# Kernel optimization log

Measured on AMD Instinct MI355X. Metric: run time of the kernel, lower is better.

Reference implementation:

```python
import jax, jax.numpy as jnp
import numpy as np

HEADS = 4
DIM_HEAD = 32
DIM = 256
EPS = 1e-12


def setup_inputs() -> dict:
    key = jax.random.key(0)
    ks = jax.random.split(key, 4)
    b, c, n = 8, DIM, 16384
    hidden = HEADS * DIM_HEAD  # 128
    x = jax.random.normal(ks[0], (b, c, n), dtype=jnp.float32)
    w_qkv = jax.random.normal(ks[1], (hidden * 3, c), dtype=jnp.float32) * (1.0 / np.sqrt(c))
    w_out = jax.random.normal(ks[2], (c, hidden), dtype=jnp.float32) * (1.0 / np.sqrt(hidden))
    b_out = jax.random.normal(ks[3], (c,), dtype=jnp.float32) * 0.01
    g = jnp.ones((1, c, 1), dtype=jnp.float32)
    return {"x": x, "w_qkv": w_qkv, "w_out": w_out, "b_out": b_out, "g": g}


def reference(x, w_qkv, w_out, b_out, g):
    b, c, n = x.shape
    scale = DIM_HEAD ** -0.5
    # to_qkv: Conv1d kernel-size 1, no bias == channel matmul
    qkv = jnp.einsum('oc,bcn->bon', w_qkv, x)  # [b, 3*h*d, n]
    q, k, v = jnp.split(qkv, 3, axis=1)
    def to_heads(t):
        return t.reshape(b, HEADS, DIM_HEAD, n)  # b (h d) n -> b h d n
    q, k, v = to_heads(q), to_heads(k), to_heads(v)
    q = jax.nn.softmax(q, axis=-2) * scale      # softmax over d
    k = jax.nn.softmax(k, axis=-1)              # softmax over n
    context = jnp.einsum('bhdn,bhen->bhde', k, v)  # [b,h,d,e]
    out = jnp.einsum('bhde,bhdn->bhen', context, q)  # [b,h,e,n]
    out = out.reshape(b, HEADS * DIM_HEAD, n)   # b h d n -> b (h d) n
    # to_out Conv1d (kernel 1) with bias
    out = jnp.einsum('oc,bcn->bon', w_out, out) + b_out[None, :, None]
    # RMSNorm: F.normalize over channel dim * g * sqrt(c)
    norm = jnp.sqrt(jnp.sum(out * out, axis=1, keepdims=True))
    out = out / jnp.maximum(norm, EPS) * g * jnp.sqrt(jnp.asarray(c, out.dtype))
    return out
```

## Files before the change

kernel.cpp:

```cpp
#include <hip/hip_runtime.h>
#include <hip/hip_bf16.h>
#include <math.h>

#define B_    8
#define C_    256
#define N_    16384
#define H_    4
#define D_    32
#define HID_  128
#define ROWS_ 384
#define SCALE 0.17677669529663687f

typedef __attribute__((ext_vector_type(8))) short bf16x8;
typedef __attribute__((ext_vector_type(16))) float f32x16;

__device__ __forceinline__ short f2bf(float f) {
    union { __hip_bfloat16 h; short s; } u;
    u.h = __float2bfloat16(f);
    return u.s;
}
__device__ __forceinline__ float bf2f(short s) {
    union { unsigned u; float f; } x;
    x.u = ((unsigned)(unsigned short)s) << 16;
    return x.f;
}

__global__ __launch_bounds__(256) void k_conv(
    const float* __restrict__ wqkv, const float* __restrict__ wout,
    short* __restrict__ wrearr, short* __restrict__ woutb)
{
    int i = blockIdx.x * 256 + threadIdx.x;
    if (i < 12288) {
        int tile = i >> 10;
        int ks   = (i >> 6) & 15;
        int l    = i & 63;
        int row  = tile * 32 + (l & 31);
        int k0   = ks * 16 + (l >> 5) * 8;
        const float* src = wqkv + row * 256 + k0;
        float4 f0 = *(const float4*)(src);
        float4 f1 = *(const float4*)(src + 4);
        short o[8] = {f2bf(f0.x), f2bf(f0.y), f2bf(f0.z), f2bf(f0.w),
                      f2bf(f1.x), f2bf(f1.y), f2bf(f1.z), f2bf(f1.w)};
        *(uint4*)(wrearr + (size_t)i * 8) = *(uint4*)o;
    } else {
        int j = (i - 12288) * 4;
        float4 f = *(const float4*)(wout + j);
        short4 s; s.x = f2bf(f.x); s.y = f2bf(f.y); s.z = f2bf(f.z); s.w = f2bf(f.w);
        *(short4*)(woutb + j) = s;
    }
}

__global__ __launch_bounds__(512, 4) void k_qkv(
    const float* __restrict__ x, const short* __restrict__ wrearr,
    short* __restrict__ qtb, short* __restrict__ part16,
    float* __restrict__ partden)
{
    __shared__ __align__(16) char smA[65536];

    const int orig = blockIdx.x;
    const int swz  = (orig & 7) * 128 + (orig >> 3);
    const int b    = swz >> 7;
    const int nwin = swz & 127;
    const int nb   = nwin << 7;
    const int t    = threadIdx.x;
    const int l    = t & 63;
    const int wv   = t >> 6;
    const int h    = wv & 3;
    const int ch   = wv >> 2;
    const int c31  = l & 31;
    const int hf   = l >> 5;

    {
        const int kg = t >> 5;
        const int n4 = (t & 31) * 4;
        const float* xb = x + (size_t)b * C_ * N_ + nb + n4;
#pragma unroll
        for (int it = 0; it < 4; it++) {
            const int k = it * 64 + kg * 4;
            const float* xp = xb + (size_t)k * N_;
            float4 r0 = *(const float4*)(xp);
            float4 r1 = *(const float4*)(xp + N_);
            float4 r2 = *(const float4*)(xp + 2 * (size_t)N_);
            float4 r3 = *(const float4*)(xp + 3 * (size_t)N_);
#define WRT(J, FLD) { short4 sv; sv.x = f2bf(r0.FLD); sv.y = f2bf(r1.FLD); \
    sv.z = f2bf(r2.FLD); sv.w = f2bf(r3.FLD); \
    int n_ = n4 + J; int ad_ = n_ * 512 + ((2 * k) ^ ((n_ & 31) << 4)); \
    *(short4*)(smA + ad_) = sv; }
            WRT(0, x) WRT(1, y) WRT(2, z) WRT(3, w)
#undef WRT
        }
    }
    __syncthreads();

    f32x16 acc[3][2];
#pragma unroll
    for (int ti = 0; ti < 3; ti++)
#pragma unroll
        for (int ct = 0; ct < 2; ct++)
#pragma unroll
            for (int r = 0; r < 16; r++) acc[ti][ct][r] = 0.f;

    const bf16x8* wp = (const bf16x8*)wrearr + (size_t)h * 1024 + l;
    bf16x8 afN0 = wp[0], afN1 = wp[4096], afN2 = wp[8192];
    const char* smB0 = smA + (ch * 64 + c31) * 512;
    const char* smB1 = smA + (ch * 64 + 32 + c31) * 512;
#pragma unroll
    for (int ks = 0; ks < 16; ks++) {
        bf16x8 af0 = afN0, af1 = afN1, af2 = afN2;
        if (ks < 15) {
            afN0 = wp[(ks + 1) * 64];
            afN1 = wp[4096 + (ks + 1) * 64];
            afN2 = wp[8192 + (ks + 1) * 64];
        }
        const int slot = 2 * ks + hf;
        bf16x8 bfr0 = *(const bf16x8*)(smB0 + 16 * (slot ^ c31));
        bf16x8 bfr1 = *(const bf16x8*)(smB1 + 16 * (slot ^ c31));
        acc[0][0] = __builtin_amdgcn_mfma_f32_32x32x16_bf16(af0, bfr0, acc[0][0], 0, 0, 0);
        acc[0][1] = __builtin_amdgcn_mfma_f32_32x32x16_bf16(af0, bfr1, acc[0][1], 0, 0, 0);
        acc[1][0] = __builtin_amdgcn_mfma_f32_32x32x16_bf16(af1, bfr0, acc[1][0], 0, 0, 0);
        acc[1][1] = __builtin_amdgcn_mfma_f32_32x32x16_bf16(af1, bfr1, acc[1][1], 0, 0, 0);
        acc[2][0] = __builtin_amdgcn_mfma_f32_32x32x16_bf16(af2, bfr0, acc[2][0], 0, 0, 0);
        acc[2][1] = __builtin_amdgcn_mfma_f32_32x32x16_bf16(af2, bfr1, acc[2][1], 0, 0, 0);
    }


#pragma unroll
    for (int ct = 0; ct < 2; ct++) {
        float mx = -1e30f;
#pragma unroll
        for (int r = 0; r < 16; r++) mx = fmaxf(mx, acc[0][ct][r]);
        mx = fmaxf(mx, __shfl_xor(mx, 32));
        float e[16]; float s = 0.f;
#pragma unroll
        for (int r = 0; r < 16; r++) { e[r] = __expf(acc[0][ct][r] - mx); s += e[r]; }
        s += __shfl_xor(s, 32);
        float inv = SCALE / s;
        short* qp = qtb + ((size_t)b * HID_ + h * 32) * N_ + nb + ch * 64 + ct * 32 + c31;
#pragma unroll
        for (int r = 0; r < 16; r++) {
            int rm = (r & 3) + 8 * (r >> 2) + 4 * hf;
            qp[(size_t)rm * N_] = f2bf(e[r] * inv);
        }
    }
    __syncthreads();

    char* ekb = smA + wv * 8192;
    char* vvb = ekb + 4096;
#pragma unroll
    for (int ct = 0; ct < 2; ct++)
#pragma unroll
        for (int r = 0; r < 16; r++) {
            int rm = (r & 3) + 8 * (r >> 2) + 4 * hf;
            int n  = ct * 32 + c31;
            int ad = rm * 128 + ((2 * n) ^ ((rm & 7) << 4));
            *(short*)(ekb + ad) = f2bf(__expf(acc[1][ct][r]));
            *(short*)(vvb + ad) = f2bf(acc[2][ct][r]);
        }

    f32x16 cD, dD;
#pragma unroll
    for (int r = 0; r < 16; r++) { cD[r] = 0.f; dD[r] = 0.f; }
    bf16x8 ones;
#pragma unroll
    for (int i = 0; i < 8; i++) ones[i] = (short)0x3F80;
#pragma unroll
    for (int ks = 0; ks < 4; ks++) {
        int slot = 2 * ks + hf;
        bf16x8 ea = *(const bf16x8*)(ekb + c31 * 128 + 16 * (slot ^ (c31 & 7)));
        bf16x8 vb = *(const bf16x8*)(vvb + c31 * 128 + 16 * (slot ^ (c31 & 7)));
        cD = __builtin_amdgcn_mfma_f32_32x32x16_bf16(ea, vb,   cD, 0, 0, 0);
        dD = __builtin_amdgcn_mfma_f32_32x32x16_bf16(ea, ones, dD, 0, 0, 0);
    }

    const int q64 = nwin * 2 + ch;
    short* pb = part16 + ((size_t)(b * 256 + q64) * 4 + h) * 1024;
#pragma unroll
    for (int r = 0; r < 16; r++) {
        int rm = (r & 3) + 8 * (r >> 2) + 4 * hf;
        pb[rm * 32 + c31] = f2bf(cD[r]);
    }
    if (c31 == 0) {
        float* pd = partden + ((size_t)(b * 256 + q64) * 4 + h) * 32;
#pragma unroll
        for (int r = 0; r < 16; r++) {
            int rm = (r & 3) + 8 * (r >> 2) + 4 * hf;
            pd[rm] = dD[r];
        }
    }
}

__global__ __launch_bounds__(256) void k_red(
    const short* __restrict__ part16, const float* __restrict__ partden,
    short* __restrict__ ctxbf)
{
    __shared__ float den_s[32];
    const int bh = blockIdx.x;
    const int b  = bh >> 2, h = bh & 3;
    const int t  = threadIdx.x;
    const int d  = t >> 3;
    const int e4 = (t & 7) * 4;

    const short* p0 = part16 + ((size_t)(b * 256) * 4 + h) * 1024 + d * 32 + e4;
    float s0 = 0.f, s1 = 0.f, s2 = 0.f, s3 = 0.f;
    for (int q = 0; q < 256; q++) {
        short4 v = *(const short4*)(p0 + (size_t)q * 4096);
        s0 += bf2f(v.x); s1 += bf2f(v.y); s2 += bf2f(v.z); s3 += bf2f(v.w);
    }
    if ((t & 7) == 0) {
        const float* pd = partden + ((size_t)(b * 256) * 4 + h) * 32 + d;
        float ds = 0.f;
        for (int q = 0; q < 256; q++) ds += pd[(size_t)q * 128];
        den_s[d] = ds;
    }
    __syncthreads();
    float inv = 1.0f / den_s[d];
    short* cb = ctxbf + (size_t)bh * 1024 + d;
    cb[(e4 + 0) * 32] = f2bf(s0 * inv);
    cb[(e4 + 1) * 32] = f2bf(s1 * inv);
    cb[(e4 + 2) * 32] = f2bf(s2 * inv);
    cb[(e4 + 3) * 32] = f2bf(s3 * inv);
}

__global__ __launch_bounds__(256, 3) void k_out(
    const short* __restrict__ qtb, const short* __restrict__ ctxbf,
    const short* __restrict__ woutb, const float* __restrict__ bout,
    const float* __restrict__ g, float* __restrict__ out)
{
    __shared__ __align__(16) char  hidS[16384];
    __shared__ float gl[C_], bl[C_];
    __shared__ float red[4][64];
    __shared__ float nrm[64];

    const int blk = blockIdx.x;
    const int b   = blk >> 8;
    const int n0  = (blk & 255) << 6;
    const int t   = threadIdx.x;
    const int l   = t & 63;
    const int wv  = t >> 6;
    const int c31 = l & 31;
    const int hf  = l >> 5;

    gl[t] = g[t];
    bl[t] = bout[t];
    __syncthreads();

    f32x16 hD[2];
#pragma unroll
    for (int ct = 0; ct < 2; ct++)
#pragma unroll
        for (int r = 0; r < 16; r++) hD[ct][r] = 0.f;
    const short* qb = qtb + (size_t)b * HID_ * N_ + n0;
    const short* cb = ctxbf + ((size_t)(b * H_ + wv) * 32 + c31) * 32;
#pragma unroll
    for (int ks = 0; ks < 2; ks++) {
        int k0 = ks * 16 + hf * 8;
        bf16x8 af = *(const bf16x8*)(cb + k0);
#pragma unroll
        for (int ct = 0; ct < 2; ct++) {
            bf16x8 bq;
#pragma unroll
            for (int i = 0; i < 8; i++)
                bq[i] = qb[(size_t)(wv * 32 + k0 + i) * N_ + ct * 32 + c31];
            hD[ct] = __builtin_amdgcn_mfma_f32_32x32x16_bf16(af, bq, hD[ct], 0, 0, 0);
        }
    }
#pragma unroll
    for (int ct = 0; ct < 2; ct++)
#pragma unroll
        for (int r = 0; r < 16; r++) {
            int rm = (r & 3) + 8 * (r >> 2) + 4 * hf;
            int hfull = wv * 32 + rm;
            int n = ct * 32 + c31;
            int ad = n * 256 + ((2 * hfull) ^ ((n & 15) << 4));
            *(short*)(hidS + ad) = f2bf(hD[ct][r]);
        }
    __syncthreads();

    f32x16 yacc[2][2];
#pragma unroll
    for (int rt = 0; rt < 2; rt++)
#pragma unroll
        for (int ct = 0; ct < 2; ct++)
#pragma unroll
            for (int r = 0; r < 16; r++) yacc[rt][ct][r] = 0.f;

#pragma unroll
    for (int ks = 0; ks < 8; ks++) {
        int k0 = ks * 16 + hf * 8;
        int sx = 2 * ks + hf;
        bf16x8 bq0 = *(const bf16x8*)(hidS + (c31)      * 256 + 16 * (sx ^ (c31 & 15)));
        bf16x8 bq1 = *(const bf16x8*)(hidS + (c31 + 32) * 256 + 16 * (sx ^ (c31 & 15)));
#pragma unroll
        for (int rt = 0; rt < 2; rt++) {
            bf16x8 af = *(const bf16x8*)(woutb + (wv * 64 + rt * 32 + c31) * HID_ + k0);
            yacc[rt][0] = __builtin_amdgcn_mfma_f32_32x32x16_bf16(af, bq0, yacc[rt][0], 0, 0, 0);
            yacc[rt][1] = __builtin_amdgcn_mfma_f32_32x32x16_bf16(af, bq1, yacc[rt][1], 0, 0, 0);
        }
    }

#pragma unroll
    for (int rt = 0; rt < 2; rt++)
#pragma unroll
        for (int r = 0; r < 16; r++) {
            int rm = (r & 3) + 8 * (r >> 2) + 4 * hf;
            float bo = bl[wv * 64 + rt * 32 + rm];
            yacc[rt][0][r] += bo;
            yacc[rt][1][r] += bo;
        }
#pragma unroll
    for (int ct = 0; ct < 2; ct++) {
        float s = 0.f;
#pragma unroll
        for (int rt = 0; rt < 2; rt++)
#pragma unroll
            for (int r = 0; r < 16; r++) s = fmaf(yacc[rt][ct][r], yacc[rt][ct][r], s);
        s += __shfl_xor(s, 32);
        if (hf == 0) red[wv][ct * 32 + c31] = s;
    }
    __syncthreads();
    if (t < 64) {
        float S = red[0][t] + red[1][t] + red[2][t] + red[3][t];
        nrm[t] = 16.0f / fmaxf(sqrtf(S), 1e-12f);
    }
    __syncthreads();

    float* ob = out + (size_t)b * C_ * N_ + n0;
#pragma unroll
    for (int rt = 0; rt < 2; rt++)
#pragma unroll
        for (int r = 0; r < 16; r++) {
            int rm = (r & 3) + 8 * (r >> 2) + 4 * hf;
            int c  = wv * 64 + rt * 32 + rm;
            float gc = gl[c];
#pragma unroll
            for (int ct = 0; ct < 2; ct++) {
                int n = ct * 32 + c31;
                ob[(size_t)c * N_ + n] = yacc[rt][ct][r] * gc * nrm[n];
            }
        }
}

extern "C" void kernel_launch(void* const* d_in, const int* in_sizes, int n_in,
                              void* d_out, int out_size, void* d_ws, size_t ws_size,
                              hipStream_t stream)
{
    const float* x    = (const float*)d_in[0];
    const float* wqkv = (const float*)d_in[1];
    const float* wout = (const float*)d_in[2];
    const float* bout = (const float*)d_in[3];
    const float* g    = (const float*)d_in[4];
    float* out = (float*)d_out;

    short* qtb     = (short*)d_ws;
    short* part16  = qtb + (size_t)B_ * N_ * HID_;
    float* partden = (float*)(part16 + (size_t)2048 * 4 * 1024);
    short* ctxbf   = (short*)(partden + (size_t)2048 * 4 * 32);
    short* wrearr  = ctxbf + (size_t)B_ * H_ * 32 * 32;
    short* woutb   = wrearr + (size_t)12288 * 8;

    k_conv<<<80, 256, 0, stream>>>(wqkv, wout, wrearr, woutb);
    k_qkv<<<1024, 512, 0, stream>>>(x, wrearr, qtb, part16, partden);
    k_red<<<B_ * H_, 256, 0, stream>>>(part16, partden, ctxbf);
    k_out<<<B_ * (N_ / 64), 256, 0, stream>>>(qtb, ctxbf, woutb, bout, g, out);
}
```

Before: 137.4 us.

## Stage x tiles via global_load_lds and use nontemporal output stores

Replaces the direct register load of x in k_qkv with chunked async global-to-LDS copies into an fp32 staging buffer, followed by a bf16 conversion into the swizzled MMA image. Launch bounds occupancy hint drops from 4 to 2 blocks because LDS use grows by 16KB. Output stores in the final kernel become nontemporal to avoid cache pollution. This adds two barriers per chunk (16 total) and lower occupancy in exchange for the more direct global-to-LDS load path.

```diff
diff --git a/kernel.cpp b/kernel.cpp
--- a/kernel.cpp
+++ b/kernel.cpp
@@ -50,12 +50,13 @@
     }
 }
 
-__global__ __launch_bounds__(512, 4) void k_qkv(
+__global__ __launch_bounds__(512, 2) void k_qkv(
     const float* __restrict__ x, const short* __restrict__ wrearr,
     short* __restrict__ qtb, short* __restrict__ part16,
     float* __restrict__ partden)
 {
-    __shared__ __align__(16) char smA[65536];
+    __shared__ __align__(16) char  img[65536];
+    __shared__ __align__(16) float xf[32 * 128];
 
     const int orig = blockIdx.x;
     const int swz  = (orig & 7) * 128 + (orig >> 3);
@@ -71,26 +72,38 @@
     const int hf   = l >> 5;
 
     {
-        const int kg = t >> 5;
-        const int n4 = (t & 31) * 4;
-        const float* xb = x + (size_t)b * C_ * N_ + nb + n4;
-#pragma unroll
-        for (int it = 0; it < 4; it++) {
-            const int k = it * 64 + kg * 4;
-            const float* xp = xb + (size_t)k * N_;
-            float4 r0 = *(const float4*)(xp);
-            float4 r1 = *(const float4*)(xp + N_);
-            float4 r2 = *(const float4*)(xp + 2 * (size_t)N_);
-            float4 r3 = *(const float4*)(xp + 3 * (size_t)N_);
-#define WRT(J, FLD) { short4 sv; sv.x = f2bf(r0.FLD); sv.y = f2bf(r1.FLD); \
-    sv.z = f2bf(r2.FLD); sv.w = f2bf(r3.FLD); \
-    int n_ = n4 + J; int ad_ = n_ * 512 + ((2 * k) ^ ((n_ & 31) << 4)); \
-    *(short4*)(smA + ad_) = sv; }
-            WRT(0, x) WRT(1, y) WRT(2, z) WRT(3, w)
-#undef WRT
-        }
-    }
-    __syncthreads();
+        const float* xg = x + (size_t)b * C_ * N_ + nb + (l & 31) * 4;
+        const int cvn  = t & 127;
+        const int cvkq = t >> 7;
+        const float* xcol = xf + cvn;
+        char* imgn = img + cvn * 512;
+        const int swm = (cvn & 31) << 4;
+
+        for (int c = 0; c < 8; c++) {
+#pragma unroll
+            for (int j = 0; j < 2; j++) {
+                const int krow = (j * 8 + wv) * 2 + hf;
+                const int kglob = c * 32 + krow;
+                __builtin_amdgcn_global_load_lds(
+                    (const __attribute__((address_space(1))) void*)(xg + (size_t)kglob * N_),
+                    (__attribute__((address_space(3))) void*)((char*)xf + (j * 8 + wv) * 1024),
+                    16, 0, 0);
+            }
+            __syncthreads();
+#pragma unroll
+            for (int p = 0; p < 4; p++) {
+                const int kl = cvkq * 8 + p * 2;
+                float f0 = xcol[(size_t)kl * 128];
+                float f1 = xcol[(size_t)(kl + 1) * 128];
+                const int kglob = c * 32 + kl;
+                ushort2 v;
+                v.x = (unsigned short)f2bf(f0);
+                v.y = (unsigned short)f2bf(f1);
+                *(ushort2*)(imgn + ((2 * kglob) ^ swm)) = v;
+            }
+            __syncthreads();
+        }
+    }
 
     f32x16 acc[3][2];
 #pragma unroll
@@ -102,8 +115,8 @@
 
     const bf16x8* wp = (const bf16x8*)wrearr + (size_t)h * 1024 + l;
     bf16x8 afN0 = wp[0], afN1 = wp[4096], afN2 = wp[8192];
-    const char* smB0 = smA + (ch * 64 + c31) * 512;
-    const char* smB1 = smA + (ch * 64 + 32 + c31) * 512;
+    const char* smB0 = img + (ch * 64 + c31) * 512;
+    const char* smB1 = img + (ch * 64 + 32 + c31) * 512;
 #pragma unroll
     for (int ks = 0; ks < 16; ks++) {
         bf16x8 af0 = afN0, af1 = afN1, af2 = afN2;
@@ -144,7 +157,7 @@
     }
     __syncthreads();
 
-    char* ekb = smA + wv * 8192;
+    char* ekb = img + wv * 8192;
     char* vvb = ekb + 4096;
 #pragma unroll
     for (int ct = 0; ct < 2; ct++)
@@ -335,7 +348,8 @@
 #pragma unroll
             for (int ct = 0; ct < 2; ct++) {
                 int n = ct * 32 + c31;
-                ob[(size_t)c * N_ + n] = yacc[rt][ct][r] * gc * nrm[n];
+                __builtin_nontemporal_store(yacc[rt][ct][r] * gc * nrm[n],
+                                            &ob[(size_t)c * N_ + n]);
             }
         }
 }
```

Result: faster. 134.4 us (-2.2%).

## Pre-convert x to bf16 in a separate pass and use nontemporal output stores

Applied to the files above, without the earlier changes.

Adds a standalone kernel that converts the whole fp32 input x to bf16, storing it in the output buffer as scratch. The QKV kernel then loads bf16 values instead of converting fp32 on the fly. The final output writes become nontemporal stores. This adds an extra full pass over x (read fp32, write bf16) to make the QKV kernel's loads cheaper. That makes total traffic higher overall, and the scheme relies on the output buffer being safe to reuse as scratch before k_out overwrites it.

```diff
diff --git a/kernel.cpp b/kernel.cpp
--- a/kernel.cpp
+++ b/kernel.cpp
@@ -50,12 +50,23 @@
     }
 }
 
+__global__ __launch_bounds__(256) void k_xcvt(
+    const float* __restrict__ x, short* __restrict__ xbf)
+{
+    size_t i = ((size_t)blockIdx.x * 256 + threadIdx.x) * 8;
+    float4 a = *(const float4*)(x + i);
+    float4 b = *(const float4*)(x + i + 4);
+    short o[8] = {f2bf(a.x), f2bf(a.y), f2bf(a.z), f2bf(a.w),
+                  f2bf(b.x), f2bf(b.y), f2bf(b.z), f2bf(b.w)};
+    *(uint4*)(xbf + i) = *(uint4*)o;
+}
+
 __global__ __launch_bounds__(512, 4) void k_qkv(
-    const float* __restrict__ x, const short* __restrict__ wrearr,
+    const short* __restrict__ xbf, const short* __restrict__ wrearr,
     short* __restrict__ qtb, short* __restrict__ part16,
     float* __restrict__ partden)
 {
-    __shared__ __align__(16) char smA[65536];
+    __shared__ __align__(16) char img[65536];
 
     const int orig = blockIdx.x;
     const int swz  = (orig & 7) * 128 + (orig >> 3);
@@ -73,19 +84,19 @@
     {
         const int kg = t >> 5;
         const int n4 = (t & 31) * 4;
-        const float* xb = x + (size_t)b * C_ * N_ + nb + n4;
+        const short* xb = xbf + (size_t)b * C_ * N_ + nb + n4;
 #pragma unroll
         for (int it = 0; it < 4; it++) {
             const int k = it * 64 + kg * 4;
-            const float* xp = xb + (size_t)k * N_;
-            float4 r0 = *(const float4*)(xp);
-            float4 r1 = *(const float4*)(xp + N_);
-            float4 r2 = *(const float4*)(xp + 2 * (size_t)N_);
-            float4 r3 = *(const float4*)(xp + 3 * (size_t)N_);
-#define WRT(J, FLD) { short4 sv; sv.x = f2bf(r0.FLD); sv.y = f2bf(r1.FLD); \
-    sv.z = f2bf(r2.FLD); sv.w = f2bf(r3.FLD); \
+            const short* xp = xb + (size_t)k * N_;
+            ushort4 r0 = *(const ushort4*)(xp);
+            ushort4 r1 = *(const ushort4*)(xp + N_);
+            ushort4 r2 = *(const ushort4*)(xp + 2 * (size_t)N_);
+            ushort4 r3 = *(const ushort4*)(xp + 3 * (size_t)N_);
+#define WRT(J, FLD) { ushort4 sv; sv.x = r0.FLD; sv.y = r1.FLD; \
+    sv.z = r2.FLD; sv.w = r3.FLD; \
     int n_ = n4 + J; int ad_ = n_ * 512 + ((2 * k) ^ ((n_ & 31) << 4)); \
-    *(short4*)(smA + ad_) = sv; }
+    *(ushort4*)(img + ad_) = sv; }
             WRT(0, x) WRT(1, y) WRT(2, z) WRT(3, w)
 #undef WRT
         }
@@ -102,8 +113,8 @@
 
     const bf16x8* wp = (const bf16x8*)wrearr + (size_t)h * 1024 + l;
     bf16x8 afN0 = wp[0], afN1 = wp[4096], afN2 = wp[8192];
-    const char* smB0 = smA + (ch * 64 + c31) * 512;
-    const char* smB1 = smA + (ch * 64 + 32 + c31) * 512;
+    const char* smB0 = img + (ch * 64 + c31) * 512;
+    const char* smB1 = img + (ch * 64 + 32 + c31) * 512;
 #pragma unroll
     for (int ks = 0; ks < 16; ks++) {
         bf16x8 af0 = afN0, af1 = afN1, af2 = afN2;
@@ -144,7 +155,7 @@
     }
     __syncthreads();
 
-    char* ekb = smA + wv * 8192;
+    char* ekb = img + wv * 8192;
     char* vvb = ekb + 4096;
 #pragma unroll
     for (int ct = 0; ct < 2; ct++)
@@ -335,7 +346,8 @@
 #pragma unroll
             for (int ct = 0; ct < 2; ct++) {
                 int n = ct * 32 + c31;
-                ob[(size_t)c * N_ + n] = yacc[rt][ct][r] * gc * nrm[n];
+                __builtin_nontemporal_store(yacc[rt][ct][r] * gc * nrm[n],
+                                            &ob[(size_t)c * N_ + n]);
             }
         }
 }
@@ -351,6 +363,8 @@
     const float* g    = (const float*)d_in[4];
     float* out = (float*)d_out;
 
+    short* xbf     = (short*)d_out;
+
     short* qtb     = (short*)d_ws;
     short* part16  = qtb + (size_t)B_ * N_ * HID_;
     float* partden = (float*)(part16 + (size_t)2048 * 4 * 1024);
@@ -359,7 +373,8 @@
     short* woutb   = wrearr + (size_t)12288 * 8;
 
     k_conv<<<80, 256, 0, stream>>>(wqkv, wout, wrearr, woutb);
-    k_qkv<<<1024, 512, 0, stream>>>(x, wrearr, qtb, part16, partden);
+    k_xcvt<<<16384, 256, 0, stream>>>(x, xbf);
+    k_qkv<<<1024, 512, 0, stream>>>(xbf, wrearr, qtb, part16, partden);
     k_red<<<B_ * H_, 256, 0, stream>>>(part16, partden, ctxbf);
     k_out<<<B_ * (N_ / 64), 256, 0, stream>>>(qtb, ctxbf, woutb, bout, g, out);
 }
```

Result: slower. 145.9 us (+6.2%).
